# Optimization experiments

Measured on AMD Instinct MI355X. Metric: run time of the kernel, lower is better.

The kernel has to match this reference:

```python
import jax, jax.numpy as jnp
import numpy as np

B, N, C = 32, 8732, 81  # batch, SSD300 anchors, COCO classes incl. background


def setup_inputs() -> dict:
    key = jax.random.key(0)
    k1, k2, k3, k4, k5 = jax.random.split(key, 5)
    ploc = jax.random.normal(k1, (B, N, 4), jnp.float32)
    plabel = jax.random.normal(k2, (B, N, C), jnp.float32)
    gloc = jax.random.normal(k3, (B, N, 4), jnp.float32)
    labels = jax.random.randint(k4, (B, N), 1, C)
    is_pos = jax.random.uniform(k5, (B, N)) < 0.02
    glabel = jnp.where(is_pos, labels, 0).astype(jnp.int32)
    return {"ploc": ploc, "plabel": plabel, "gloc": gloc, "glabel": glabel}


def _smooth_l1(x):
    ax = jnp.abs(x)
    return jnp.where(ax < 1.0, 0.5 * ax * ax, ax - 0.5)


def reference(ploc, plabel, gloc, glabel):
    num_classes = plabel.shape[-1]
    mask = glabel.reshape(-1) > 0                      # [B*N] positive anchors
    pos_num = mask.sum()

    # Localization loss: SmoothL1 summed over 4 coords, only on positives
    loss_l = _smooth_l1(ploc.reshape(-1, 4) - gloc.reshape(-1, 4)).sum(axis=1)
    loss_l = (mask.astype(loss_l.dtype) * loss_l).sum()

    # Per-anchor cross entropy over flattened batch
    logp = jax.nn.log_softmax(plabel.reshape(-1, num_classes), axis=-1)
    gt = glabel.reshape(-1)
    loss_c = -jnp.take_along_axis(logp, gt[:, None], axis=1)[:, 0]  # [B*N]

    # Hard negative mining via double argsort (rank of each anchor's CE loss)
    con_neg = jnp.where(mask, 0.0, loss_c)
    con_idx = jnp.argsort(-con_neg)        # descending sort indices
    con_rank = jnp.argsort(con_idx)        # rank of each element
    neg_num = jnp.minimum(3 * pos_num, mask.shape[0])
    neg_mask = con_rank < neg_num

    closs = (loss_c * (mask.astype(loss_c.dtype) + neg_mask.astype(loss_c.dtype))).sum()
    total_loss = loss_l + closs
    return jnp.where(pos_num > 0, total_loss / pos_num.astype(total_loss.dtype), 0.0)
```

## Files before the change

kernel.cpp:

```cpp
#include <hip/hip_runtime.h>
#include <math.h>

#define M_TOTAL (32 * 8732)
#define NBLK_A  (M_TOTAL / 64)
#define NREP    32
#define NH1     273

#define CON_B    ((size_t)0)
#define HISTR_B  ((size_t)M_TOTAL * 4)
#define H1_B     (HISTR_B + (size_t)NREP * 2048 * 4)
#define H2_B     (H1_B + (size_t)2048 * 4)
#define G_B      (H2_B + (size_t)1024 * 4)
#define PART_B   (G_B + 64)
#define ZERO_BYTES ((H2_B + 1024 * 4 + 64) - HISTR_B)

struct GS {
    unsigned pn;
    float    lossl;
    float    poslc;
    unsigned b0;
    unsigned k1;
    unsigned pref;
    unsigned k2;
    float    sumhi0;
    float    sumhi1;
};

__device__ __forceinline__ float smooth_l1(float d) {
    float ad = fabsf(d);
    return (ad < 1.0f) ? 0.5f * ad * ad : ad - 0.5f;
}

#define GLLDS16(gp, lp) __builtin_amdgcn_global_load_lds( \
    (__attribute__((address_space(1))) void*)(gp),        \
    (__attribute__((address_space(3))) void*)(lp), 16, 0, 0)

__global__ __launch_bounds__(256) void kA(const float* __restrict__ ploc,
                                          const float* __restrict__ plabel,
                                          const float* __restrict__ gloc,
                                          const int* __restrict__ glabel,
                                          float* __restrict__ con,
                                          unsigned* __restrict__ histR,
                                          float4* __restrict__ part) {
    __shared__ __align__(16) float stage[4 * 1296];
    __shared__ unsigned lh[2048];
    __shared__ float    rf[4][3];

    const int tid  = threadIdx.x;
    const int w    = tid >> 6;
    const int lane = tid & 63;
    const int g    = lane >> 2;
    const int l    = lane & 3;

    for (int i = tid; i < 2048; i += 256) lh[i] = 0u;

    const size_t wrow0 = (size_t)blockIdx.x * 64 + (size_t)w * 16;
    const char*  gsrc  = (const char*)(plabel + wrow0 * 81);
    char*        ldst  = (char*)&stage[w * 1296];
#pragma unroll
    for (int j = 0; j < 5; ++j)
        GLLDS16(gsrc + (size_t)j * 1024 + (size_t)lane * 16, ldst + j * 1024);
    if (lane < 4)
        GLLDS16(gsrc + 5120 + (size_t)lane * 16, ldst + 5120);

    const size_t row = wrow0 + g;
    const float pl = ploc[wrow0 * 4 + lane];
    const float gl = gloc[wrow0 * 4 + lane];
    int gt = 0;
    if (l == 0) gt = glabel[row];
    const int mask = gt > 0;

    float s = smooth_l1(pl - gl);
    s += __shfl_xor(s, 1);
    s += __shfl_xor(s, 2);

    __syncthreads();

    const float* rowp = &stage[w * 1296 + g * 81];
    float v[20];
    float m = -INFINITY;
#pragma unroll
    for (int j = 0; j < 20; ++j) { v[j] = rowp[j * 4 + l]; m = fmaxf(m, v[j]); }
    float v80 = 0.0f;
    if (l == 0) { v80 = rowp[80]; m = fmaxf(m, v80); }
    m = fmaxf(m, __shfl_xor(m, 1));
    m = fmaxf(m, __shfl_xor(m, 2));

    float e = 0.0f;
#pragma unroll
    for (int j = 0; j < 20; ++j) e += __expf(v[j] - m);
    if (l == 0) e += __expf(v80 - m);
    e += __shfl_xor(e, 1);
    e += __shfl_xor(e, 2);
    const float lse = m + __logf(e);

    float wl = 0.f, wc = 0.f, wp = 0.f;
    if (l == 0) {
        const float x_gt   = rowp[gt];
        const float loss_c = lse - x_gt;
        const float cn     = mask ? 0.0f : fmaxf(loss_c, 0.0f);
        con[row] = cn;
        atomicAdd(&lh[__float_as_uint(cn) >> 21], 1u);
        if (mask) { wl = s; wc = loss_c; wp = 1.0f; }
    }
#pragma unroll
    for (int off = 4; off < 64; off <<= 1) {
        wl += __shfl_xor(wl, off);
        wc += __shfl_xor(wc, off);
        wp += __shfl_xor(wp, off);
    }
    if (lane == 0) { rf[w][0] = wl; rf[w][1] = wc; rf[w][2] = wp; }
    __syncthreads();

    if (tid == 0)
        part[blockIdx.x] = make_float4(rf[0][0] + rf[1][0] + rf[2][0] + rf[3][0],
                                       rf[0][1] + rf[1][1] + rf[2][1] + rf[3][1],
                                       rf[0][2] + rf[1][2] + rf[2][2] + rf[3][2], 0.f);

    unsigned* hrep = histR + (size_t)(blockIdx.x & (NREP - 1)) * 2048;
    for (int i = tid; i < 2048; i += 256) {
        const unsigned c = lh[i];
        if (c) atomicAdd(&hrep[i], c);
    }
}

__device__ void suffix_select(const unsigned* h, int nbins, unsigned k,
                              unsigned* ssum, unsigned* pbin, unsigned* pk) {
    const int t = threadIdx.x;
    if (t == 0) { *pbin = 0u; *pk = 0u; }
    const unsigned h0 = (2 * t     < nbins) ? h[2 * t]     : 0u;
    const unsigned h1 = (2 * t + 1 < nbins) ? h[2 * t + 1] : 0u;
    ssum[t] = h0 + h1;
    __syncthreads();
    for (int off = 1; off < 1024; off <<= 1) {
        const unsigned val = ssum[t];
        const unsigned add = (t + off < 1024) ? ssum[t + off] : 0u;
        __syncthreads();
        ssum[t] = val + add;
        __syncthreads();
    }
    const unsigned sA = ssum[t];
    const unsigned sB = sA - h0;
    const unsigned sC = (t + 1 < 1024) ? ssum[t + 1] : 0u;
    if (k > 0u) {
        if (2 * t < nbins && sA >= k && k > sB) { *pbin = 2u * (unsigned)t;      *pk = k - sB; }
        if (2 * t + 1 < nbins && sB >= k && k > sC) { *pbin = 2u * (unsigned)t + 1u; *pk = k - sC; }
    }
    __syncthreads();
}

__global__ __launch_bounds__(1024) void kR0(const unsigned* __restrict__ histR,
                                            const float4* __restrict__ part,
                                            GS* __restrict__ G) {
    __shared__ unsigned lh[2048];
    __shared__ unsigned ssum[1024];
    __shared__ float    rf3[16][3];
    __shared__ unsigned sbin, sk;
    const int t = threadIdx.x;

    for (int b = t; b < 2048; b += 1024) {
        unsigned c = 0;
#pragma unroll
        for (int r = 0; r < NREP; ++r) c += histR[r * 2048 + b];
        lh[b] = c;
    }

    float sl = 0.f, sc = 0.f, sp = 0.f;
    for (int i = t; i < NBLK_A; i += 1024) {
        const float4 p = part[i];
        sl += p.x; sc += p.y; sp += p.z;
    }
#pragma unroll
    for (int off = 1; off < 64; off <<= 1) {
        sl += __shfl_xor(sl, off); sc += __shfl_xor(sc, off); sp += __shfl_xor(sp, off);
    }
    if ((t & 63) == 0) { rf3[t >> 6][0] = sl; rf3[t >> 6][1] = sc; rf3[t >> 6][2] = sp; }
    __syncthreads();

    float tsl = 0.f, tsc = 0.f, tsp = 0.f;
    for (int i = 0; i < 16; ++i) { tsl += rf3[i][0]; tsc += rf3[i][1]; tsp += rf3[i][2]; }
    const unsigned pn = (unsigned)(tsp + 0.5f);
    unsigned k0 = 3u * pn;
    if (k0 > (unsigned)M_TOTAL) k0 = (unsigned)M_TOTAL;

    suffix_select(lh, 2048, k0, ssum, &sbin, &sk);
    if (t == 0) {
        G->pn = pn; G->lossl = tsl; G->poslc = tsc;
        G->b0 = sbin; G->k1 = sk;
    }
}

__global__ __launch_bounds__(256) void kH1(const float4* __restrict__ con4,
                                           unsigned* __restrict__ h1,
                                           GS* __restrict__ G) {
    __shared__ float wred[4];
    const unsigned b0 = G->b0;
    const int i = blockIdx.x * 256 + threadIdx.x;
    float s = 0.f;
    if (i < M_TOTAL / 4) {
        const float4 q = con4[i];
        const float xs[4] = {q.x, q.y, q.z, q.w};
#pragma unroll
        for (int j = 0; j < 4; ++j) {
            const unsigned u  = __float_as_uint(xs[j]);
            const unsigned hi = u >> 21;
            if (hi > b0) s += xs[j];
            else if (hi == b0) atomicAdd(&h1[(u >> 10) & 0x7FFu], 1u);
        }
    }
#pragma unroll
    for (int off = 1; off < 64; off <<= 1) s += __shfl_xor(s, off);
    if ((threadIdx.x & 63) == 0) wred[threadIdx.x >> 6] = s;
    __syncthreads();
    if (threadIdx.x == 0) {
        const float tot = wred[0] + wred[1] + wred[2] + wred[3];
        if (tot != 0.f) atomicAdd(&G->sumhi0, tot);
    }
}

__global__ __launch_bounds__(1024) void kR1(const unsigned* __restrict__ h1,
                                            GS* __restrict__ G) {
    __shared__ unsigned ssum[1024];
    __shared__ unsigned sbin, sk;
    const unsigned k1 = G->k1;
    suffix_select(h1, 2048, k1, ssum, &sbin, &sk);
    if (threadIdx.x == 0) {
        G->pref = (G->b0 << 11) | sbin;
        G->k2   = sk;
    }
}

__global__ __launch_bounds__(256) void kH2(const float4* __restrict__ con4,
                                           unsigned* __restrict__ h2,
                                           GS* __restrict__ G) {
    __shared__ float wred[4];
    const unsigned pref = G->pref;
    const unsigned b0 = pref >> 11, b1 = pref & 0x7FFu;
    const int i = blockIdx.x * 256 + threadIdx.x;
    float s = 0.f;
    if (i < M_TOTAL / 4) {
        const float4 q = con4[i];
        const float xs[4] = {q.x, q.y, q.z, q.w};
#pragma unroll
        for (int j = 0; j < 4; ++j) {
            const unsigned u = __float_as_uint(xs[j]);
            if ((u >> 21) == b0) {
                const unsigned mid = (u >> 10) & 0x7FFu;
                if (mid > b1) s += xs[j];
                else if (mid == b1) atomicAdd(&h2[u & 0x3FFu], 1u);
            }
        }
    }
#pragma unroll
    for (int off = 1; off < 64; off <<= 1) s += __shfl_xor(s, off);
    if ((threadIdx.x & 63) == 0) wred[threadIdx.x >> 6] = s;
    __syncthreads();
    if (threadIdx.x == 0) {
        const float tot = wred[0] + wred[1] + wred[2] + wred[3];
        if (tot != 0.f) atomicAdd(&G->sumhi1, tot);
    }
}

__global__ __launch_bounds__(1024) void kR2(const unsigned* __restrict__ h2,
                                            const GS* __restrict__ G,
                                            float* __restrict__ out) {
    __shared__ unsigned lh[1024];
    __shared__ unsigned ssum[1024];
    __shared__ unsigned sbin, sk;
    __shared__ float    wred[16];
    const int t = threadIdx.x;
    const unsigned k2   = G->k2;
    const unsigned pref = G->pref;

    const unsigned c = h2[t];
    lh[t] = c;
    __syncthreads();
    suffix_select(lh, 1024, k2, ssum, &sbin, &sk);
    const unsigned ct = sbin, r = sk;

    float s = 0.f;
    if ((unsigned)t > ct && c)
        s = (float)c * __uint_as_float((pref << 10) | (unsigned)t);
#pragma unroll
    for (int off = 1; off < 64; off <<= 1) s += __shfl_xor(s, off);
    if ((t & 63) == 0) wred[t >> 6] = s;
    __syncthreads();

    if (t == 0) {
        float sumhi2 = 0.f;
        for (int i = 0; i < 16; ++i) sumhi2 += wred[i];
        const unsigned pn = G->pn;
        float outv = 0.f;
        if (pn > 0u) {
            const float tval  = __uint_as_float((pref << 10) | ct);
            const float closs = G->poslc + G->sumhi0 + G->sumhi1 + sumhi2 + (float)r * tval;
            outv = (G->lossl + closs) / (float)pn;
        }
        out[0] = outv;
    }
}

extern "C" void kernel_launch(void* const* d_in, const int* in_sizes, int n_in,
                              void* d_out, int out_size, void* d_ws, size_t ws_size,
                              hipStream_t stream) {
    const float* ploc   = (const float*)d_in[0];
    const float* plabel = (const float*)d_in[1];
    const float* gloc   = (const float*)d_in[2];
    const int*   glabel = (const int*)d_in[3];
    float* out = (float*)d_out;
    char*  ws  = (char*)d_ws;

    float*    con   = (float*)(ws + CON_B);
    unsigned* histR = (unsigned*)(ws + HISTR_B);
    unsigned* h1    = (unsigned*)(ws + H1_B);
    unsigned* h2    = (unsigned*)(ws + H2_B);
    GS*       G     = (GS*)(ws + G_B);
    float4*   part  = (float4*)(ws + PART_B);

    hipMemsetAsync(ws + HISTR_B, 0, ZERO_BYTES, stream);

    kA <<<NBLK_A, 256, 0, stream>>>(ploc, plabel, gloc, glabel, con, histR, part);
    kR0<<<1, 1024, 0, stream>>>(histR, part, G);
    kH1<<<NH1, 256, 0, stream>>>((const float4*)con, h1, G);
    kR1<<<1, 1024, 0, stream>>>(h1, G);
    kH2<<<NH1, 256, 0, stream>>>((const float4*)con, h2, G);
    kR2<<<1, 1024, 0, stream>>>(h2, G, out);
}
```

Measured before the change: 181.4 us.

## Fuse single-block select kernels into last-block epilogues and drop memset

Replaces the six-kernel pipeline plus memset with four kernels. The three single-block 1024-thread radix-select kernels become last-block-done epilogues of the scan kernels, using atomic counters and threadfences. Workspace zeroing moves into the first kernel, the coarse histogram moves out of kA into a separate pass over con, and the replica count drops from 32 to 8. The aim is to remove launch gaps and serialized tiny kernels, at the cost of one extra read pass over con and added atomic/fence overhead.

```diff
diff --git a/kernel.cpp b/kernel.cpp
--- a/kernel.cpp
+++ b/kernel.cpp
@@ -2,17 +2,18 @@
 #include <math.h>
 
 #define M_TOTAL (32 * 8732)
+#define M4      (M_TOTAL / 4)
 #define NBLK_A  (M_TOTAL / 64)
-#define NREP    32
-#define NH1     273
+#define NBLK_S  273
+#define NREP    8
 
 #define CON_B    ((size_t)0)
 #define HISTR_B  ((size_t)M_TOTAL * 4)
 #define H1_B     (HISTR_B + (size_t)NREP * 2048 * 4)
 #define H2_B     (H1_B + (size_t)2048 * 4)
 #define G_B      (H2_B + (size_t)1024 * 4)
-#define PART_B   (G_B + 64)
-#define ZERO_BYTES ((H2_B + 1024 * 4 + 64) - HISTR_B)
+#define PART_B   (G_B + 128)
+#define ZERO_WORDS ((NREP * 2048 * 4 + 2048 * 4 + 1024 * 4 + 128) / 4)
 
 struct GS {
     unsigned pn;
@@ -24,27 +25,62 @@
     unsigned k2;
     float    sumhi0;
     float    sumhi1;
+    unsigned ctrB, ctrC, ctrD;
 };
 
 __device__ __forceinline__ float smooth_l1(float d) {
     float ad = fabsf(d);
     return (ad < 1.0f) ? 0.5f * ad * ad : ad - 0.5f;
 }
+__device__ __forceinline__ unsigned aload(const unsigned* p) {
+    return __hip_atomic_load(p, __ATOMIC_RELAXED, __HIP_MEMORY_SCOPE_AGENT);
+}
+__device__ __forceinline__ float aloadf(const float* p) {
+    return __hip_atomic_load(p, __ATOMIC_RELAXED, __HIP_MEMORY_SCOPE_AGENT);
+}
 
 #define GLLDS16(gp, lp) __builtin_amdgcn_global_load_lds( \
     (__attribute__((address_space(1))) void*)(gp),        \
     (__attribute__((address_space(3))) void*)(lp), 16, 0, 0)
+
+__device__ void selectk256(const unsigned* cnt, int nbins, unsigned k,
+                           unsigned* ssum, unsigned* pbin, unsigned* pk) {
+    const int t = threadIdx.x;
+    const int chunk = nbins >> 8;
+    if (t == 0) { *pbin = 0u; *pk = 0u; }
+    unsigned tot = 0;
+    for (int j = 0; j < chunk; ++j) tot += cnt[t * chunk + j];
+    ssum[t] = tot;
+    __syncthreads();
+    for (int off = 1; off < 256; off <<= 1) {
+        const unsigned val = ssum[t];
+        const unsigned add = (t + off < 256) ? ssum[t + off] : 0u;
+        __syncthreads();
+        ssum[t] = val + add;
+        __syncthreads();
+    }
+    const unsigned s_after = (t < 255) ? ssum[t + 1] : 0u;
+    if (k > 0u && ssum[t] >= k && k > s_after) {
+        unsigned cum = s_after;
+        for (int j = chunk - 1; j >= 0; --j) {
+            const unsigned bin = t * chunk + j;
+            const unsigned nc = cum + cnt[bin];
+            if (nc >= k) { *pbin = bin; *pk = k - cum; break; }
+            cum = nc;
+        }
+    }
+    __syncthreads();
+}
 
 __global__ __launch_bounds__(256) void kA(const float* __restrict__ ploc,
                                           const float* __restrict__ plabel,
                                           const float* __restrict__ gloc,
                                           const int* __restrict__ glabel,
                                           float* __restrict__ con,
-                                          unsigned* __restrict__ histR,
+                                          unsigned* __restrict__ zbase,
                                           float4* __restrict__ part) {
     __shared__ __align__(16) float stage[4 * 1296];
-    __shared__ unsigned lh[2048];
-    __shared__ float    rf[4][3];
+    __shared__ float rf[4][3];
 
     const int tid  = threadIdx.x;
     const int w    = tid >> 6;
@@ -52,7 +88,10 @@
     const int g    = lane >> 2;
     const int l    = lane & 3;
 
-    for (int i = tid; i < 2048; i += 256) lh[i] = 0u;
+    if (blockIdx.x < 77) {
+        const int zi = blockIdx.x * 256 + tid;
+        if (zi < ZERO_WORDS) zbase[zi] = 0u;
+    }
 
     const size_t wrow0 = (size_t)blockIdx.x * 64 + (size_t)w * 16;
     const char*  gsrc  = (const char*)(plabel + wrow0 * 81);
@@ -100,7 +139,6 @@
         const float loss_c = lse - x_gt;
         const float cn     = mask ? 0.0f : fmaxf(loss_c, 0.0f);
         con[row] = cn;
-        atomicAdd(&lh[__float_as_uint(cn) >> 21], 1u);
         if (mask) { wl = s; wc = loss_c; wp = 1.0f; }
     }
 #pragma unroll
@@ -116,88 +154,88 @@
         part[blockIdx.x] = make_float4(rf[0][0] + rf[1][0] + rf[2][0] + rf[3][0],
                                        rf[0][1] + rf[1][1] + rf[2][1] + rf[3][1],
                                        rf[0][2] + rf[1][2] + rf[2][2] + rf[3][2], 0.f);
+}
+
+__global__ __launch_bounds__(256) void kB(const float4* __restrict__ con4,
+                                          unsigned* __restrict__ histR,
+                                          const float4* __restrict__ part,
+                                          GS* __restrict__ G) {
+    __shared__ unsigned lh[2048];
+    __shared__ unsigned ssum[256];
+    __shared__ unsigned sbin, sk;
+    __shared__ float    rf3[4][3];
+    __shared__ int      amLast;
+    const int tid = threadIdx.x;
+
+    for (int i = tid; i < 2048; i += 256) lh[i] = 0u;
+    __syncthreads();
+
+    const int i = blockIdx.x * 256 + tid;
+    if (i < M4) {
+        const float4 q = con4[i];
+        atomicAdd(&lh[__float_as_uint(q.x) >> 21], 1u);
+        atomicAdd(&lh[__float_as_uint(q.y) >> 21], 1u);
+        atomicAdd(&lh[__float_as_uint(q.z) >> 21], 1u);
+        atomicAdd(&lh[__float_as_uint(q.w) >> 21], 1u);
+    }
+    __syncthreads();
 
     unsigned* hrep = histR + (size_t)(blockIdx.x & (NREP - 1)) * 2048;
-    for (int i = tid; i < 2048; i += 256) {
-        const unsigned c = lh[i];
-        if (c) atomicAdd(&hrep[i], c);
-    }
-}
-
-__device__ void suffix_select(const unsigned* h, int nbins, unsigned k,
-                              unsigned* ssum, unsigned* pbin, unsigned* pk) {
-    const int t = threadIdx.x;
-    if (t == 0) { *pbin = 0u; *pk = 0u; }
-    const unsigned h0 = (2 * t     < nbins) ? h[2 * t]     : 0u;
-    const unsigned h1 = (2 * t + 1 < nbins) ? h[2 * t + 1] : 0u;
-    ssum[t] = h0 + h1;
-    __syncthreads();
-    for (int off = 1; off < 1024; off <<= 1) {
-        const unsigned val = ssum[t];
-        const unsigned add = (t + off < 1024) ? ssum[t + off] : 0u;
-        __syncthreads();
-        ssum[t] = val + add;
-        __syncthreads();
-    }
-    const unsigned sA = ssum[t];
-    const unsigned sB = sA - h0;
-    const unsigned sC = (t + 1 < 1024) ? ssum[t + 1] : 0u;
-    if (k > 0u) {
-        if (2 * t < nbins && sA >= k && k > sB) { *pbin = 2u * (unsigned)t;      *pk = k - sB; }
-        if (2 * t + 1 < nbins && sB >= k && k > sC) { *pbin = 2u * (unsigned)t + 1u; *pk = k - sC; }
-    }
-    __syncthreads();
-}
-
-__global__ __launch_bounds__(1024) void kR0(const unsigned* __restrict__ histR,
-                                            const float4* __restrict__ part,
-                                            GS* __restrict__ G) {
-    __shared__ unsigned lh[2048];
-    __shared__ unsigned ssum[1024];
-    __shared__ float    rf3[16][3];
-    __shared__ unsigned sbin, sk;
-    const int t = threadIdx.x;
-
-    for (int b = t; b < 2048; b += 1024) {
+    for (int b = tid; b < 2048; b += 256) {
+        const unsigned c = lh[b];
+        if (c) atomicAdd(&hrep[b], c);
+    }
+
+    __threadfence();
+    if (tid == 0) amLast = (atomicAdd(&G->ctrB, 1u) == (unsigned)(gridDim.x - 1));
+    __syncthreads();
+    if (!amLast) return;
+
+    for (int b = tid; b < 2048; b += 256) {
         unsigned c = 0;
 #pragma unroll
-        for (int r = 0; r < NREP; ++r) c += histR[r * 2048 + b];
+        for (int r = 0; r < NREP; ++r) c += aload(&histR[r * 2048 + b]);
         lh[b] = c;
     }
-
     float sl = 0.f, sc = 0.f, sp = 0.f;
-    for (int i = t; i < NBLK_A; i += 1024) {
-        const float4 p = part[i];
-        sl += p.x; sc += p.y; sp += p.z;
+    for (int p = tid; p < NBLK_A; p += 256) {
+        const float4 q = part[p];
+        sl += q.x; sc += q.y; sp += q.z;
     }
 #pragma unroll
     for (int off = 1; off < 64; off <<= 1) {
         sl += __shfl_xor(sl, off); sc += __shfl_xor(sc, off); sp += __shfl_xor(sp, off);
     }
-    if ((t & 63) == 0) { rf3[t >> 6][0] = sl; rf3[t >> 6][1] = sc; rf3[t >> 6][2] = sp; }
-    __syncthreads();
-
-    float tsl = 0.f, tsc = 0.f, tsp = 0.f;
-    for (int i = 0; i < 16; ++i) { tsl += rf3[i][0]; tsc += rf3[i][1]; tsp += rf3[i][2]; }
+    if ((tid & 63) == 0) { rf3[tid >> 6][0] = sl; rf3[tid >> 6][1] = sc; rf3[tid >> 6][2] = sp; }
+    __syncthreads();
+    const float tsl = rf3[0][0] + rf3[1][0] + rf3[2][0] + rf3[3][0];
+    const float tsc = rf3[0][1] + rf3[1][1] + rf3[2][1] + rf3[3][1];
+    const float tsp = rf3[0][2] + rf3[1][2] + rf3[2][2] + rf3[3][2];
     const unsigned pn = (unsigned)(tsp + 0.5f);
     unsigned k0 = 3u * pn;
     if (k0 > (unsigned)M_TOTAL) k0 = (unsigned)M_TOTAL;
 
-    suffix_select(lh, 2048, k0, ssum, &sbin, &sk);
-    if (t == 0) {
+    selectk256(lh, 2048, k0, ssum, &sbin, &sk);
+    if (tid == 0) {
         G->pn = pn; G->lossl = tsl; G->poslc = tsc;
         G->b0 = sbin; G->k1 = sk;
     }
 }
 
-__global__ __launch_bounds__(256) void kH1(const float4* __restrict__ con4,
-                                           unsigned* __restrict__ h1,
-                                           GS* __restrict__ G) {
-    __shared__ float wred[4];
+__global__ __launch_bounds__(256) void kC(const float4* __restrict__ con4,
+                                          unsigned* __restrict__ h1,
+                                          GS* __restrict__ G) {
+    __shared__ unsigned lh[2048];
+    __shared__ unsigned ssum[256];
+    __shared__ unsigned sbin, sk;
+    __shared__ float    wred[4];
+    __shared__ int      amLast;
+    const int tid = threadIdx.x;
+
     const unsigned b0 = G->b0;
-    const int i = blockIdx.x * 256 + threadIdx.x;
+    const int i = blockIdx.x * 256 + tid;
     float s = 0.f;
-    if (i < M_TOTAL / 4) {
+    if (i < M4) {
         const float4 q = con4[i];
         const float xs[4] = {q.x, q.y, q.z, q.w};
 #pragma unroll
@@ -210,35 +248,44 @@
     }
 #pragma unroll
     for (int off = 1; off < 64; off <<= 1) s += __shfl_xor(s, off);
-    if ((threadIdx.x & 63) == 0) wred[threadIdx.x >> 6] = s;
-    __syncthreads();
-    if (threadIdx.x == 0) {
+    if ((tid & 63) == 0) wred[tid >> 6] = s;
+    __syncthreads();
+    if (tid == 0) {
         const float tot = wred[0] + wred[1] + wred[2] + wred[3];
         if (tot != 0.f) atomicAdd(&G->sumhi0, tot);
     }
-}
-
-__global__ __launch_bounds__(1024) void kR1(const unsigned* __restrict__ h1,
-                                            GS* __restrict__ G) {
-    __shared__ unsigned ssum[1024];
+
+    __threadfence();
+    if (tid == 0) amLast = (atomicAdd(&G->ctrC, 1u) == (unsigned)(gridDim.x - 1));
+    __syncthreads();
+    if (!amLast) return;
+
+    for (int b = tid; b < 2048; b += 256) lh[b] = aload(&h1[b]);
+    __syncthreads();
+    const unsigned k1 = G->k1;
+    selectk256(lh, 2048, k1, ssum, &sbin, &sk);
+    if (tid == 0) {
+        G->pref = (b0 << 11) | sbin;
+        G->k2   = sk;
+    }
+}
+
+__global__ __launch_bounds__(256) void kD(const float4* __restrict__ con4,
+                                          unsigned* __restrict__ h2,
+                                          GS* __restrict__ G,
+                                          float* __restrict__ out) {
+    __shared__ unsigned lh[1024];
+    __shared__ unsigned ssum[256];
     __shared__ unsigned sbin, sk;
-    const unsigned k1 = G->k1;
-    suffix_select(h1, 2048, k1, ssum, &sbin, &sk);
-    if (threadIdx.x == 0) {
-        G->pref = (G->b0 << 11) | sbin;
-        G->k2   = sk;
-    }
-}
-
-__global__ __launch_bounds__(256) void kH2(const float4* __restrict__ con4,
-                                           unsigned* __restrict__ h2,
-                                           GS* __restrict__ G) {
-    __shared__ float wred[4];
+    __shared__ float    wred[4];
+    __shared__ int      amLast;
+    const int tid = threadIdx.x;
+
     const unsigned pref = G->pref;
     const unsigned b0 = pref >> 11, b1 = pref & 0x7FFu;
-    const int i = blockIdx.x * 256 + threadIdx.x;
+    const int i = blockIdx.x * 256 + tid;
     float s = 0.f;
-    if (i < M_TOTAL / 4) {
+    if (i < M4) {
         const float4 q = con4[i];
         const float xs[4] = {q.x, q.y, q.z, q.w};
 #pragma unroll
@@ -253,47 +300,43 @@
     }
 #pragma unroll
     for (int off = 1; off < 64; off <<= 1) s += __shfl_xor(s, off);
-    if ((threadIdx.x & 63) == 0) wred[threadIdx.x >> 6] = s;
-    __syncthreads();
-    if (threadIdx.x == 0) {
+    if ((tid & 63) == 0) wred[tid >> 6] = s;
+    __syncthreads();
+    if (tid == 0) {
         const float tot = wred[0] + wred[1] + wred[2] + wred[3];
         if (tot != 0.f) atomicAdd(&G->sumhi1, tot);
     }
-}
-
-__global__ __launch_bounds__(1024) void kR2(const unsigned* __restrict__ h2,
-                                            const GS* __restrict__ G,
-                                            float* __restrict__ out) {
-    __shared__ unsigned lh[1024];
-    __shared__ unsigned ssum[1024];
-    __shared__ unsigned sbin, sk;
-    __shared__ float    wred[16];
-    const int t = threadIdx.x;
-    const unsigned k2   = G->k2;
-    const unsigned pref = G->pref;
-
-    const unsigned c = h2[t];
-    lh[t] = c;
-    __syncthreads();
-    suffix_select(lh, 1024, k2, ssum, &sbin, &sk);
+
+    __threadfence();
+    if (tid == 0) amLast = (atomicAdd(&G->ctrD, 1u) == (unsigned)(gridDim.x - 1));
+    __syncthreads();
+    if (!amLast) return;
+
+    for (int b = tid; b < 1024; b += 256) lh[b] = aload(&h2[b]);
+    __syncthreads();
+    const unsigned k2 = G->k2;
+    selectk256(lh, 1024, k2, ssum, &sbin, &sk);
     const unsigned ct = sbin, r = sk;
 
-    float s = 0.f;
-    if ((unsigned)t > ct && c)
-        s = (float)c * __uint_as_float((pref << 10) | (unsigned)t);
-#pragma unroll
-    for (int off = 1; off < 64; off <<= 1) s += __shfl_xor(s, off);
-    if ((t & 63) == 0) wred[t >> 6] = s;
-    __syncthreads();
-
-    if (t == 0) {
-        float sumhi2 = 0.f;
-        for (int i = 0; i < 16; ++i) sumhi2 += wred[i];
+    float s2 = 0.f;
+    for (int b = tid; b < 1024; b += 256) {
+        const unsigned c = lh[b];
+        if ((unsigned)b > ct && c)
+            s2 += (float)c * __uint_as_float((pref << 10) | (unsigned)b);
+    }
+#pragma unroll
+    for (int off = 1; off < 64; off <<= 1) s2 += __shfl_xor(s2, off);
+    if ((tid & 63) == 0) wred[tid >> 6] = s2;
+    __syncthreads();
+
+    if (tid == 0) {
+        const float sumhi2 = wred[0] + wred[1] + wred[2] + wred[3];
         const unsigned pn = G->pn;
         float outv = 0.f;
         if (pn > 0u) {
             const float tval  = __uint_as_float((pref << 10) | ct);
-            const float closs = G->poslc + G->sumhi0 + G->sumhi1 + sumhi2 + (float)r * tval;
+            const float sumhi1 = aloadf(&G->sumhi1);
+            const float closs = G->poslc + G->sumhi0 + sumhi1 + sumhi2 + (float)r * tval;
             outv = (G->lossl + closs) / (float)pn;
         }
         out[0] = outv;
@@ -317,12 +360,9 @@
     GS*       G     = (GS*)(ws + G_B);
     float4*   part  = (float4*)(ws + PART_B);
 
-    hipMemsetAsync(ws + HISTR_B, 0, ZERO_BYTES, stream);
-
-    kA <<<NBLK_A, 256, 0, stream>>>(ploc, plabel, gloc, glabel, con, histR, part);
-    kR0<<<1, 1024, 0, stream>>>(histR, part, G);
-    kH1<<<NH1, 256, 0, stream>>>((const float4*)con, h1, G);
-    kR1<<<1, 1024, 0, stream>>>(h1, G);
-    kH2<<<NH1, 256, 0, stream>>>((const float4*)con, h2, G);
-    kR2<<<1, 1024, 0, stream>>>(h2, G, out);
-}
+    kA<<<NBLK_A, 256, 0, stream>>>(ploc, plabel, gloc, glabel, con,
+                                   (unsigned*)(ws + HISTR_B), part);
+    kB<<<NBLK_S, 256, 0, stream>>>((const float4*)con, histR, part, G);
+    kC<<<NBLK_S, 256, 0, stream>>>((const float4*)con, h1, G);
+    kD<<<NBLK_S, 256, 0, stream>>>((const float4*)con, h2, G, out);
+}
```

New measurement: 226.3 us. 24.7% more time.
